# Kernel optimization log

Hardware: AMD Instinct MI355X
Metric: run time of the kernel (lower is better)

Reference implementation:

```python
import jax, jax.numpy as jnp
import numpy as np

N_EMBD = 1024  # C; source scales scores by C**-0.5 (n_embd, not head_size)


def setup_inputs() -> dict:
    key = jax.random.key(0)
    kx, kk, kq, kv = jax.random.split(key, 4)
    B, T, C, H = 8, 2048, N_EMBD, 64
    x = jax.random.normal(kx, (B, T, C), dtype=jnp.float32)
    Wk = jax.random.normal(kk, (C, H), dtype=jnp.float32) * (C ** -0.5)
    Wq = jax.random.normal(kq, (C, H), dtype=jnp.float32) * (C ** -0.5)
    Wv = jax.random.normal(kv, (C, H), dtype=jnp.float32) * (C ** -0.5)
    return {"x": x, "Wk": Wk, "Wq": Wq, "Wv": Wv}


def reference(x, Wk, Wq, Wv):
    B, T, C = x.shape
    k = jnp.einsum('btc,ch->bth', x, Wk)
    q = jnp.einsum('btc,ch->bth', x, Wq)
    v = jnp.einsum('btc,ch->bth', x, Wv)
    # scores scaled by C**-0.5 (faithful to source, which uses n_embd not head_size)
    wei = jnp.einsum('bth,bsh->bts', q, k) * (C ** -0.5)  # [B,T,T]
    causal = jnp.tril(jnp.ones((T, T), dtype=bool))
    wei = jnp.where(causal, wei, -jnp.inf)
    wei = jax.nn.softmax(wei, axis=-1)
    # dropout is identity in eval mode
    out = jnp.einsum('bts,bsh->bth', wei, v)
    return out
```

## Files before the change

### kernel.cpp

```cpp
#include <hip/hip_runtime.h>


#define B_ 8
#define T_ 2048
#define C_ 1024
#define H_ 64
#define BTH (B_ * T_ * H_)

typedef unsigned short u16;
typedef float f32x4 __attribute__((ext_vector_type(4)));
typedef __bf16 bf16x8 __attribute__((ext_vector_type(8)));
#define AS1 __attribute__((address_space(1)))
#define AS3 __attribute__((address_space(3)))

__device__ __forceinline__ u16 f2bf(float f) {
  union { float f; unsigned u; } c; c.f = f;
  unsigned u = c.u;
  return (u16)((u + 0x7FFFu + ((u >> 16) & 1u)) >> 16);
}

__device__ __forceinline__ bf16x8 cvt8(const float4 a, const float4 b) {
  bf16x8 r;
  r[0] = (__bf16)a.x; r[1] = (__bf16)a.y; r[2] = (__bf16)a.z; r[3] = (__bf16)a.w;
  r[4] = (__bf16)b.x; r[5] = (__bf16)b.y; r[6] = (__bf16)b.z; r[7] = (__bf16)b.w;
  return r;
}

__global__ __launch_bounds__(256)
void wpack(const float* __restrict__ Wk, const float* __restrict__ Wq,
           const float* __restrict__ Wv, u16* __restrict__ Wct) {
  const int g  = blockIdx.x;
  const int k0 = blockIdx.y * 64;
  const float* __restrict__ W = (g == 0) ? Wk : (g == 1) ? Wq : Wv;
#pragma unroll
  for (int it = 0; it < 16; ++it) {
    const int idx = it * 256 + threadIdx.x;
    const int kk = k0 + (idx >> 6), h = idx & 63;
    Wct[(size_t)(g * 64 + h) * C_ + kk] = f2bf(W[(size_t)kk * H_ + h]);
  }
}

__global__ __launch_bounds__(256)
void qkv_gemm(const float* __restrict__ x, const u16* __restrict__ Wct,
              u16* __restrict__ ws) {
  __shared__ u16 As[32 * 128];
  const int tid  = threadIdx.x;
  const int wave = tid >> 6, lane = tid & 63;
  const int l15 = lane & 15, quad = lane >> 4;
  const int r0 = blockIdx.x * 32;
  const int srow = tid >> 3, sseg = tid & 7;
  const float* __restrict__ xsrc = x + (size_t)(r0 + srow) * C_ + sseg * 16;
  u16* const wdst0 = As + srow * 128 + ((2 * sseg)     ^ (srow & 15)) * 8;
  u16* const wdst1 = As + srow * 128 + ((2 * sseg + 1) ^ (srow & 15)) * 8;
  const u16* __restrict__ wp = Wct + (size_t)(wave * 48 + l15) * C_ + quad * 8;
  const u16* const ard0 = As + l15 * 128;
  const u16* const ard1 = As + (16 + l15) * 128;
  const f32x4 z = {0.f, 0.f, 0.f, 0.f};
  f32x4 acc[2][3];
#pragma unroll
  for (int m = 0; m < 2; ++m)
#pragma unroll
    for (int ni = 0; ni < 3; ++ni) acc[m][ni] = z;

#pragma unroll 1
  for (int ks = 0; ks < 8; ++ks) {
    const int k0 = ks * 128;
    float4 xa0 = *(const float4*)(xsrc + k0);
    float4 xa1 = *(const float4*)(xsrc + k0 + 4);
    float4 xa2 = *(const float4*)(xsrc + k0 + 8);
    float4 xa3 = *(const float4*)(xsrc + k0 + 12);
    bf16x8 Bf[3][4];
#pragma unroll
    for (int ni = 0; ni < 3; ++ni)
#pragma unroll
      for (int f = 0; f < 4; ++f)
        Bf[ni][f] = *(const bf16x8*)(wp + (size_t)ni * 16 * C_ + k0 + f * 32);
    __syncthreads();
    *(bf16x8*)wdst0 = cvt8(xa0, xa1);
    *(bf16x8*)wdst1 = cvt8(xa2, xa3);
    __syncthreads();
#pragma unroll
    for (int f = 0; f < 4; ++f) {
      const int co = (((4 * f + quad) ^ l15) * 8);
      const bf16x8 a0 = *(const bf16x8*)(ard0 + co);
      const bf16x8 a1 = *(const bf16x8*)(ard1 + co);
#pragma unroll
      for (int ni = 0; ni < 3; ++ni) {
        acc[0][ni] = __builtin_amdgcn_mfma_f32_16x16x32_bf16(a0, Bf[ni][f], acc[0][ni], 0, 0, 0);
        acc[1][ni] = __builtin_amdgcn_mfma_f32_16x16x32_bf16(a1, Bf[ni][f], acc[1][ni], 0, 0, 0);
      }
    }
  }
  const float SCLL = 0.03125f * 1.44269504088896f;
  const int bb = r0 >> 11;
#pragma unroll
  for (int m = 0; m < 2; ++m) {
    const int rowg = r0 + m * 16;
    const int tb = (rowg & 2047) + quad * 4;
#pragma unroll
    for (int ni = 0; ni < 3; ++ni) {
      const int col = wave * 48 + ni * 16 + l15;
      const int g = col >> 6, h = col & 63;
      f32x4 a = acc[m][ni];
      if (g == 1) { a[0] *= SCLL; a[1] *= SCLL; a[2] *= SCLL; a[3] *= SCLL; }
      if (g < 2) {
        u16* op = ws + (size_t)g * BTH + (size_t)(rowg + quad * 4) * H_ + h;
#pragma unroll
        for (int r = 0; r < 4; ++r) op[(size_t)r * H_] = f2bf(a[r]);
      } else {
        uint2 pk;
        pk.x = (unsigned)f2bf(a[0]) | ((unsigned)f2bf(a[1]) << 16);
        pk.y = (unsigned)f2bf(a[2]) | ((unsigned)f2bf(a[3]) << 16);
        *(uint2*)(ws + (size_t)2 * BTH + (size_t)(bb * H_ + h) * T_ + tb) = pk;
      }
    }
  }
}

__global__ __launch_bounds__(256)
void flash(const u16* __restrict__ ws, float* __restrict__ fpart) {
  __shared__ u16 Ks[2][64 * 64];
  __shared__ u16 Vs[2][64 * 64];
  __shared__ __bf16 Pt[4][16 * 72];
  const u16* __restrict__ kg = ws;
  const u16* __restrict__ qg = ws + BTH;
  const u16* __restrict__ vt = ws + (size_t)2 * BTH;
  const int b  = blockIdx.y;
  const int bx = 143 - (int)blockIdx.x;
  int c = 0;
#pragma unroll
  for (int t = 1; t < 8; ++t)
    if (34 * t - 2 * t * t <= bx) c = t;
  const int u = 4 * c + (bx - (34 * c - 2 * c * c));
  const int tid  = threadIdx.x;
  const int wv   = tid >> 6;
  const int lane = tid & 63;
  const int l15  = lane & 15, quad = lane >> 4;
  const int qt   = 4 * u + wv;
  const int t0   = qt * 16;
  const int st0  = 4 * c;
  const int stE  = (st0 + 4 < u + 1) ? st0 + 4 : u + 1;
  const u16* kb0 = kg + (size_t)b * T_ * H_;
  const u16* vb0 = vt + (size_t)b * H_ * T_;
  const int srow = tid >> 3, scp = tid & 7;
  const u16* qrow = qg + ((size_t)(b * T_ + t0 + l15)) * H_ + quad * 8;
  const bf16x8 qf0 = *(const bf16x8*)qrow;
  const bf16x8 qf1 = *(const bf16x8*)(qrow + 32);
  __bf16* pt = &Pt[wv][0];
  const f32x4 z = {0.f, 0.f, 0.f, 0.f};
  f32x4 o[4];
  float lr[4] = {0.f, 0.f, 0.f, 0.f};
#pragma unroll
  for (int hi = 0; hi < 4; ++hi) o[hi] = z;

  {
    const int s00 = st0 * 64;
#pragma unroll
    for (int jj = 0; jj < 2; ++jj) {
      const int row = jj * 32 + srow;
      const int sc  = scp ^ (row & 7);
      __builtin_amdgcn_global_load_lds(
          (const AS1 unsigned*)(kb0 + (size_t)(s00 + row) * H_ + sc * 8),
          (AS3 unsigned*)(&Ks[0][(jj * 256 + tid) * 8]), 16, 0, 0);
      __builtin_amdgcn_global_load_lds(
          (const AS1 unsigned*)(vb0 + (size_t)row * T_ + s00 + sc * 8),
          (AS3 unsigned*)(&Vs[0][(jj * 256 + tid) * 8]), 16, 0, 0);
    }
  }
  __syncthreads();

#pragma unroll 1
  for (int st = st0; st < stE; ++st) {
    const int cur = (st - st0) & 1;
    if (st + 1 < stE) {
      const int s1 = (st + 1) * 64;
#pragma unroll
      for (int jj = 0; jj < 2; ++jj) {
        const int row = jj * 32 + srow;
        const int sc  = scp ^ (row & 7);
        __builtin_amdgcn_global_load_lds(
            (const AS1 unsigned*)(kb0 + (size_t)(s1 + row) * H_ + sc * 8),
            (AS3 unsigned*)(&Ks[cur ^ 1][(jj * 256 + tid) * 8]), 16, 0, 0);
        __builtin_amdgcn_global_load_lds(
            (const AS1 unsigned*)(vb0 + (size_t)row * T_ + s1 + sc * 8),
            (AS3 unsigned*)(&Vs[cur ^ 1][(jj * 256 + tid) * 8]), 16, 0, 0);
      }
    }
    const u16* Kc = &Ks[cur][0];
    const u16* Vc = &Vs[cur][0];
    const int sw = (l15 & 7);
    f32x4 s[4];
#pragma unroll
    for (int ni = 0; ni < 4; ++ni) {
      const u16* kr = Kc + (ni * 16 + l15) * 64;
      const bf16x8 k0 = *(const bf16x8*)(kr + ((quad       ^ sw) * 8));
      const bf16x8 k1 = *(const bf16x8*)(kr + (((4 + quad) ^ sw) * 8));
      s[ni] = __builtin_amdgcn_mfma_f32_16x16x32_bf16(qf0, k0, z, 0, 0, 0);
      s[ni] = __builtin_amdgcn_mfma_f32_16x16x32_bf16(qf1, k1, s[ni], 0, 0, 0);
    }
    if (st == u) {
      const int s0 = st * 64;
#pragma unroll
      for (int ni = 0; ni < 4; ++ni)
#pragma unroll
        for (int r = 0; r < 4; ++r)
          if (s0 + ni * 16 + l15 > t0 + quad * 4 + r) s[ni][r] = -1e30f;
    }
    float p[4][4];
#pragma unroll
    for (int ni = 0; ni < 4; ++ni)
#pragma unroll
      for (int r = 0; r < 4; ++r) p[ni][r] = __builtin_amdgcn_exp2f(s[ni][r]);
#pragma unroll
    for (int r = 0; r < 4; ++r)
      lr[r] += (p[0][r] + p[1][r]) + (p[2][r] + p[3][r]);
#pragma unroll
    for (int ni = 0; ni < 4; ++ni)
#pragma unroll
      for (int r = 0; r < 4; ++r)
        pt[(quad * 4 + r) * 72 + ni * 16 + l15] = (__bf16)p[ni][r];
    asm volatile("s_waitcnt lgkmcnt(0)" ::: "memory");
    const bf16x8 pa0 = *(const bf16x8*)(pt + l15 * 72 + quad * 8);
    const bf16x8 pa1 = *(const bf16x8*)(pt + l15 * 72 + 32 + quad * 8);
    asm volatile("" ::: "memory");
#pragma unroll
    for (int hi = 0; hi < 4; ++hi) {
      const u16* vr = Vc + (hi * 16 + l15) * 64;
      const bf16x8 v0 = *(const bf16x8*)(vr + ((quad       ^ sw) * 8));
      const bf16x8 v1 = *(const bf16x8*)(vr + (((4 + quad) ^ sw) * 8));
      o[hi] = __builtin_amdgcn_mfma_f32_16x16x32_bf16(pa0, v0, o[hi], 0, 0, 0);
      o[hi] = __builtin_amdgcn_mfma_f32_16x16x32_bf16(pa1, v1, o[hi], 0, 0, 0);
    }
    __syncthreads();
  }
#pragma unroll
  for (int d = 1; d < 16; d <<= 1)
#pragma unroll
    for (int r = 0; r < 4; ++r) lr[r] += __shfl_xor(lr[r], d, 64);
  float* po = fpart + (size_t)((b * 128 + qt) * 8 + c) * 1040;
#pragma unroll
  for (int hi = 0; hi < 4; ++hi)
#pragma unroll
    for (int r = 0; r < 4; ++r)
      po[(quad * 4 + r) * 64 + hi * 16 + l15] = o[hi][r];
  if (l15 == 0) {
#pragma unroll
    for (int r = 0; r < 4; ++r) po[1024 + quad * 4 + r] = lr[r];
  }
}

__global__ __launch_bounds__(256)
void freduce(const float* __restrict__ fpart, float* __restrict__ out) {
  const int qt  = blockIdx.x;
  const int b   = blockIdx.y;
  const int tid = threadIdx.x;
  const int nc  = (qt >> 4) + 1;
  const float* __restrict__ pb = fpart + (size_t)(b * 128 + qt) * 8 * 1040;
  __shared__ float ls[16];
  if (tid < 16) {
    float s = 0.f;
#pragma unroll 1
    for (int i = 0; i < nc; ++i) s += pb[(size_t)i * 1040 + 1024 + tid];
    ls[tid] = s;
  }
  __syncthreads();
  f32x4 a = {0.f, 0.f, 0.f, 0.f};
#pragma unroll 1
  for (int i = 0; i < nc; ++i)
    a += *(const f32x4*)(pb + (size_t)i * 1040 + tid * 4);
  const float inv = 1.0f / ls[tid >> 4];
  a[0] *= inv; a[1] *= inv; a[2] *= inv; a[3] *= inv;
  *(f32x4*)(out + (size_t)(b * T_ + qt * 16 + (tid >> 4)) * H_ + ((tid * 4) & 63)) = a;
}

extern "C" void kernel_launch(void* const* d_in, const int* in_sizes, int n_in,
                              void* d_out, int out_size, void* d_ws, size_t ws_size,
                              hipStream_t stream) {
  const float* x  = (const float*)d_in[0];
  const float* Wk = (const float*)d_in[1];
  const float* Wq = (const float*)d_in[2];
  const float* Wv = (const float*)d_in[3];
  u16*   ws  = (u16*)d_ws;
  u16*   Wct = ws + (size_t)3 * BTH;
  float* fpart = (float*)(ws + (size_t)3 * BTH + 192 * 1024);
  float* out = (float*)d_out;
  wpack<<<dim3(3, 16), 256, 0, stream>>>(Wk, Wq, Wv, Wct);
  qkv_gemm<<<dim3(512), 256, 0, stream>>>(x, Wct, ws);
  flash<<<dim3(144, B_), 256, 0, stream>>>(ws, fpart);
  freduce<<<dim3(128, B_), 256, 0, stream>>>(fpart, out);
}
```

Measured before the change: 142.9 us.

## Double-buffer QKV GEMM LDS tile and enlarge row tile to 64

```diff
diff --git a/kernel.cpp b/kernel.cpp
--- a/kernel.cpp
+++ b/kernel.cpp
@@ -25,6 +25,12 @@
   r[4] = (__bf16)b.x; r[5] = (__bf16)b.y; r[6] = (__bf16)b.z; r[7] = (__bf16)b.w;
   return r;
 }
+
+#define GBAR() do {                                        \
+    asm volatile("s_waitcnt lgkmcnt(0)" ::: "memory");     \
+    __builtin_amdgcn_s_barrier();                          \
+    __builtin_amdgcn_sched_barrier(0);                     \
+  } while (0)
 
 __global__ __launch_bounds__(256)
 void wpack(const float* __restrict__ Wk, const float* __restrict__ Wq,
@@ -43,58 +49,106 @@
 __global__ __launch_bounds__(256)
 void qkv_gemm(const float* __restrict__ x, const u16* __restrict__ Wct,
               u16* __restrict__ ws) {
-  __shared__ u16 As[32 * 128];
+  __shared__ u16 As[2][64 * 128];
   const int tid  = threadIdx.x;
   const int wave = tid >> 6, lane = tid & 63;
   const int l15 = lane & 15, quad = lane >> 4;
-  const int r0 = blockIdx.x * 32;
-  const int srow = tid >> 3, sseg = tid & 7;
-  const float* __restrict__ xsrc = x + (size_t)(r0 + srow) * C_ + sseg * 16;
-  u16* const wdst0 = As + srow * 128 + ((2 * sseg)     ^ (srow & 15)) * 8;
-  u16* const wdst1 = As + srow * 128 + ((2 * sseg + 1) ^ (srow & 15)) * 8;
+  const int r0 = blockIdx.x * 64;
+  const int srow = tid >> 2, sseg = tid & 3;
+  const int swz = srow & 15;
+  const float* __restrict__ xsrc = x + (size_t)(r0 + srow) * C_ + sseg * 32;
+  u16* wd0[4]; u16* wd1[4];
+#pragma unroll
+  for (int jj = 0; jj < 4; ++jj) {
+    const int c = ((4 * sseg + jj) ^ swz) * 8;
+    wd0[jj] = &As[0][srow * 128 + c];
+    wd1[jj] = &As[1][srow * 128 + c];
+  }
   const u16* __restrict__ wp = Wct + (size_t)(wave * 48 + l15) * C_ + quad * 8;
-  const u16* const ard0 = As + l15 * 128;
-  const u16* const ard1 = As + (16 + l15) * 128;
   const f32x4 z = {0.f, 0.f, 0.f, 0.f};
-  f32x4 acc[2][3];
-#pragma unroll
-  for (int m = 0; m < 2; ++m)
+  f32x4 acc[4][3];
+#pragma unroll
+  for (int m = 0; m < 4; ++m)
 #pragma unroll
     for (int ni = 0; ni < 3; ++ni) acc[m][ni] = z;
 
-#pragma unroll 1
-  for (int ks = 0; ks < 8; ++ks) {
-    const int k0 = ks * 128;
-    float4 xa0 = *(const float4*)(xsrc + k0);
-    float4 xa1 = *(const float4*)(xsrc + k0 + 4);
-    float4 xa2 = *(const float4*)(xsrc + k0 + 8);
-    float4 xa3 = *(const float4*)(xsrc + k0 + 12);
-    bf16x8 Bf[3][4];
-#pragma unroll
-    for (int ni = 0; ni < 3; ++ni)
-#pragma unroll
-      for (int f = 0; f < 4; ++f)
-        Bf[ni][f] = *(const bf16x8*)(wp + (size_t)ni * 16 * C_ + k0 + f * 32);
-    __syncthreads();
-    *(bf16x8*)wdst0 = cvt8(xa0, xa1);
-    *(bf16x8*)wdst1 = cvt8(xa2, xa3);
-    __syncthreads();
-#pragma unroll
-    for (int f = 0; f < 4; ++f) {
-      const int co = (((4 * f + quad) ^ l15) * 8);
-      const bf16x8 a0 = *(const bf16x8*)(ard0 + co);
-      const bf16x8 a1 = *(const bf16x8*)(ard1 + co);
-#pragma unroll
-      for (int ni = 0; ni < 3; ++ni) {
-        acc[0][ni] = __builtin_amdgcn_mfma_f32_16x16x32_bf16(a0, Bf[ni][f], acc[0][ni], 0, 0, 0);
-        acc[1][ni] = __builtin_amdgcn_mfma_f32_16x16x32_bf16(a1, Bf[ni][f], acc[1][ni], 0, 0, 0);
-      }
+  float4 xA[8], xB[8];
+#pragma unroll
+  for (int j = 0; j < 8; ++j) xA[j] = *(const float4*)(xsrc + j * 4);
+#pragma unroll
+  for (int jj = 0; jj < 4; ++jj)
+    *(bf16x8*)wd0[jj] = cvt8(xA[2 * jj], xA[2 * jj + 1]);
+#pragma unroll
+  for (int j = 0; j < 8; ++j) xB[j] = *(const float4*)(xsrc + 128 + j * 4);
+  GBAR();
+
+#pragma unroll
+  for (int kp = 0; kp < 4; ++kp) {
+    {
+      const int k0 = (2 * kp) * 128;
+      bf16x8 Bf[3][4];
+#pragma unroll
+      for (int ni = 0; ni < 3; ++ni)
+#pragma unroll
+        for (int f = 0; f < 4; ++f)
+          Bf[ni][f] = *(const bf16x8*)(wp + (size_t)ni * 16 * C_ + k0 + f * 32);
+      if (kp < 3) {
+#pragma unroll
+        for (int j = 0; j < 8; ++j)
+          xA[j] = *(const float4*)(xsrc + k0 + 256 + j * 4);
+      }
+#pragma unroll
+      for (int f = 0; f < 4; ++f) {
+        const int co = ((4 * f + quad) ^ l15) * 8;
+#pragma unroll
+        for (int m = 0; m < 4; ++m) {
+          const bf16x8 a = *(const bf16x8*)(&As[0][(m * 16 + l15) * 128 + co]);
+#pragma unroll
+          for (int ni = 0; ni < 3; ++ni)
+            acc[m][ni] = __builtin_amdgcn_mfma_f32_16x16x32_bf16(a, Bf[ni][f], acc[m][ni], 0, 0, 0);
+        }
+      }
+#pragma unroll
+      for (int jj = 0; jj < 4; ++jj)
+        *(bf16x8*)wd1[jj] = cvt8(xB[2 * jj], xB[2 * jj + 1]);
+      GBAR();
+    }
+    {
+      const int k0 = (2 * kp + 1) * 128;
+      bf16x8 Bf[3][4];
+#pragma unroll
+      for (int ni = 0; ni < 3; ++ni)
+#pragma unroll
+        for (int f = 0; f < 4; ++f)
+          Bf[ni][f] = *(const bf16x8*)(wp + (size_t)ni * 16 * C_ + k0 + f * 32);
+      if (kp < 3) {
+#pragma unroll
+        for (int j = 0; j < 8; ++j)
+          xB[j] = *(const float4*)(xsrc + k0 + 256 + j * 4);
+      }
+#pragma unroll
+      for (int f = 0; f < 4; ++f) {
+        const int co = ((4 * f + quad) ^ l15) * 8;
+#pragma unroll
+        for (int m = 0; m < 4; ++m) {
+          const bf16x8 a = *(const bf16x8*)(&As[1][(m * 16 + l15) * 128 + co]);
+#pragma unroll
+          for (int ni = 0; ni < 3; ++ni)
+            acc[m][ni] = __builtin_amdgcn_mfma_f32_16x16x32_bf16(a, Bf[ni][f], acc[m][ni], 0, 0, 0);
+        }
+      }
+      if (kp < 3) {
+#pragma unroll
+        for (int jj = 0; jj < 4; ++jj)
+          *(bf16x8*)wd0[jj] = cvt8(xA[2 * jj], xA[2 * jj + 1]);
+      }
+      GBAR();
     }
   }
   const float SCLL = 0.03125f * 1.44269504088896f;
   const int bb = r0 >> 11;
 #pragma unroll
-  for (int m = 0; m < 2; ++m) {
+  for (int m = 0; m < 4; ++m) {
     const int rowg = r0 + m * 16;
     const int tb = (rowg & 2047) + quad * 4;
 #pragma unroll
@@ -285,7 +339,7 @@
   float* fpart = (float*)(ws + (size_t)3 * BTH + 192 * 1024);
   float* out = (float*)d_out;
   wpack<<<dim3(3, 16), 256, 0, stream>>>(Wk, Wq, Wv, Wct);
-  qkv_gemm<<<dim3(512), 256, 0, stream>>>(x, Wct, ws);
+  qkv_gemm<<<dim3(256), 256, 0, stream>>>(x, Wct, ws);
   flash<<<dim3(144, B_), 256, 0, stream>>>(ws, fpart);
   freduce<<<dim3(128, B_), 256, 0, stream>>>(fpart, out);
 }
```

Measured after the change: 139.9 us. 2.1% less time.

## Drop LDS staging in QKV GEMM, load A fragments directly with register prefetch

Applied to the files above, without the earlier changes.

```diff
diff --git a/kernel.cpp b/kernel.cpp
--- a/kernel.cpp
+++ b/kernel.cpp
@@ -43,76 +43,67 @@
 __global__ __launch_bounds__(256)
 void qkv_gemm(const float* __restrict__ x, const u16* __restrict__ Wct,
               u16* __restrict__ ws) {
-  __shared__ u16 As[32 * 128];
   const int tid  = threadIdx.x;
-  const int wave = tid >> 6, lane = tid & 63;
+  const int wv   = tid >> 6, lane = tid & 63;
   const int l15 = lane & 15, quad = lane >> 4;
-  const int r0 = blockIdx.x * 32;
-  const int srow = tid >> 3, sseg = tid & 7;
-  const float* __restrict__ xsrc = x + (size_t)(r0 + srow) * C_ + sseg * 16;
-  u16* const wdst0 = As + srow * 128 + ((2 * sseg)     ^ (srow & 15)) * 8;
-  u16* const wdst1 = As + srow * 128 + ((2 * sseg + 1) ^ (srow & 15)) * 8;
-  const u16* __restrict__ wp = Wct + (size_t)(wave * 48 + l15) * C_ + quad * 8;
-  const u16* const ard0 = As + l15 * 128;
-  const u16* const ard1 = As + (16 + l15) * 128;
+  const int ch = blockIdx.x & 1;
+  const int mt = (blockIdx.x >> 1) * 4 + wv;
+  const int r0 = mt * 16;
+  const float* __restrict__ xw = x + (size_t)(r0 + l15) * C_ + quad * 8;
+  const u16*   __restrict__ bw = Wct + (size_t)(ch * 96 + l15) * C_ + quad * 8;
   const f32x4 z = {0.f, 0.f, 0.f, 0.f};
-  f32x4 acc[2][3];
-#pragma unroll
-  for (int m = 0; m < 2; ++m)
-#pragma unroll
-    for (int ni = 0; ni < 3; ++ni) acc[m][ni] = z;
-
-#pragma unroll 1
-  for (int ks = 0; ks < 8; ++ks) {
-    const int k0 = ks * 128;
-    float4 xa0 = *(const float4*)(xsrc + k0);
-    float4 xa1 = *(const float4*)(xsrc + k0 + 4);
-    float4 xa2 = *(const float4*)(xsrc + k0 + 8);
-    float4 xa3 = *(const float4*)(xsrc + k0 + 12);
-    bf16x8 Bf[3][4];
-#pragma unroll
-    for (int ni = 0; ni < 3; ++ni)
-#pragma unroll
-      for (int f = 0; f < 4; ++f)
-        Bf[ni][f] = *(const bf16x8*)(wp + (size_t)ni * 16 * C_ + k0 + f * 32);
-    __syncthreads();
-    *(bf16x8*)wdst0 = cvt8(xa0, xa1);
-    *(bf16x8*)wdst1 = cvt8(xa2, xa3);
-    __syncthreads();
-#pragma unroll
-    for (int f = 0; f < 4; ++f) {
-      const int co = (((4 * f + quad) ^ l15) * 8);
-      const bf16x8 a0 = *(const bf16x8*)(ard0 + co);
-      const bf16x8 a1 = *(const bf16x8*)(ard1 + co);
-#pragma unroll
-      for (int ni = 0; ni < 3; ++ni) {
-        acc[0][ni] = __builtin_amdgcn_mfma_f32_16x16x32_bf16(a0, Bf[ni][f], acc[0][ni], 0, 0, 0);
-        acc[1][ni] = __builtin_amdgcn_mfma_f32_16x16x32_bf16(a1, Bf[ni][f], acc[1][ni], 0, 0, 0);
-      }
-    }
-  }
+  f32x4 acc[6];
+#pragma unroll
+  for (int ni = 0; ni < 6; ++ni) acc[ni] = z;
+
+  float4 xa0 = *(const float4*)(xw);
+  float4 xa1 = *(const float4*)(xw + 4);
+  bf16x8 bfc[6];
+#pragma unroll
+  for (int ni = 0; ni < 6; ++ni)
+    bfc[ni] = *(const bf16x8*)(bw + (size_t)ni * 16 * C_);
+
+#pragma unroll 2
+  for (int ks = 0; ks < 32; ++ks) {
+    const int k1 = (ks + 1) * 32;
+    float4 na0, na1;
+    bf16x8 bfn[6];
+    if (ks < 31) {
+      na0 = *(const float4*)(xw + k1);
+      na1 = *(const float4*)(xw + k1 + 4);
+#pragma unroll
+      for (int ni = 0; ni < 6; ++ni)
+        bfn[ni] = *(const bf16x8*)(bw + (size_t)ni * 16 * C_ + k1);
+    }
+    const bf16x8 af = cvt8(xa0, xa1);
+#pragma unroll
+    for (int ni = 0; ni < 6; ++ni)
+      acc[ni] = __builtin_amdgcn_mfma_f32_16x16x32_bf16(af, bfc[ni], acc[ni], 0, 0, 0);
+    if (ks < 31) {
+      xa0 = na0; xa1 = na1;
+#pragma unroll
+      for (int ni = 0; ni < 6; ++ni) bfc[ni] = bfn[ni];
+    }
+  }
+
   const float SCLL = 0.03125f * 1.44269504088896f;
   const int bb = r0 >> 11;
-#pragma unroll
-  for (int m = 0; m < 2; ++m) {
-    const int rowg = r0 + m * 16;
-    const int tb = (rowg & 2047) + quad * 4;
-#pragma unroll
-    for (int ni = 0; ni < 3; ++ni) {
-      const int col = wave * 48 + ni * 16 + l15;
-      const int g = col >> 6, h = col & 63;
-      f32x4 a = acc[m][ni];
-      if (g == 1) { a[0] *= SCLL; a[1] *= SCLL; a[2] *= SCLL; a[3] *= SCLL; }
-      if (g < 2) {
-        u16* op = ws + (size_t)g * BTH + (size_t)(rowg + quad * 4) * H_ + h;
-#pragma unroll
-        for (int r = 0; r < 4; ++r) op[(size_t)r * H_] = f2bf(a[r]);
-      } else {
-        uint2 pk;
-        pk.x = (unsigned)f2bf(a[0]) | ((unsigned)f2bf(a[1]) << 16);
-        pk.y = (unsigned)f2bf(a[2]) | ((unsigned)f2bf(a[3]) << 16);
-        *(uint2*)(ws + (size_t)2 * BTH + (size_t)(bb * H_ + h) * T_ + tb) = pk;
-      }
+  const int tb = (r0 & 2047) + quad * 4;
+#pragma unroll
+  for (int ni = 0; ni < 6; ++ni) {
+    const int col = ch * 96 + ni * 16 + l15;
+    const int g = col >> 6, h = col & 63;
+    f32x4 a = acc[ni];
+    if (g == 1) { a[0] *= SCLL; a[1] *= SCLL; a[2] *= SCLL; a[3] *= SCLL; }
+    if (g < 2) {
+      u16* op = ws + (size_t)g * BTH + (size_t)(r0 + quad * 4) * H_ + h;
+#pragma unroll
+      for (int r = 0; r < 4; ++r) op[(size_t)r * H_] = f2bf(a[r]);
+    } else {
+      uint2 pk;
+      pk.x = (unsigned)f2bf(a[0]) | ((unsigned)f2bf(a[1]) << 16);
+      pk.y = (unsigned)f2bf(a[2]) | ((unsigned)f2bf(a[3]) << 16);
+      *(uint2*)(ws + (size_t)2 * BTH + (size_t)(bb * H_ + h) * T_ + tb) = pk;
     }
   }
 }
```

New measurement: 172.6 us. 1.21x slower.

## Double-buffer QKV GEMM with async LDS weight loads and larger 64-row tiles

Applied to the files above, without the earlier changes.

```diff
diff --git a/kernel.cpp b/kernel.cpp
--- a/kernel.cpp
+++ b/kernel.cpp
@@ -40,21 +40,24 @@
   }
 }
 
-__global__ __launch_bounds__(256)
+__global__ __launch_bounds__(512, 1)
 void qkv_gemm(const float* __restrict__ x, const u16* __restrict__ Wct,
               u16* __restrict__ ws) {
-  __shared__ u16 As[32 * 128];
+  __shared__ u16 Bs[2][192 * 128];
+  __shared__ u16 Xs[2][64 * 128];
   const int tid  = threadIdx.x;
-  const int wave = tid >> 6, lane = tid & 63;
+  const int wv   = tid >> 6, lane = tid & 63;
   const int l15 = lane & 15, quad = lane >> 4;
-  const int r0 = blockIdx.x * 32;
-  const int srow = tid >> 3, sseg = tid & 7;
-  const float* __restrict__ xsrc = x + (size_t)(r0 + srow) * C_ + sseg * 16;
-  u16* const wdst0 = As + srow * 128 + ((2 * sseg)     ^ (srow & 15)) * 8;
-  u16* const wdst1 = As + srow * 128 + ((2 * sseg + 1) ^ (srow & 15)) * 8;
-  const u16* __restrict__ wp = Wct + (size_t)(wave * 48 + l15) * C_ + quad * 8;
-  const u16* const ard0 = As + l15 * 128;
-  const u16* const ard1 = As + (16 + l15) * 128;
+  const int wr = wv >> 2, wc = wv & 3;
+  const int r0 = blockIdx.x * 64;
+  const int xrow = tid >> 3, xcp = tid & 7;
+  const int xw0 = (xcp ^ (xrow & 7)) * 8;
+  const float* __restrict__ xsrc = x + (size_t)(r0 + xrow) * C_;
+  u16* const xd0 = &Xs[0][xrow * 128 + xw0];
+  u16* const xd1 = &Xs[1][xrow * 128 + xw0];
+  const int arow = wr * 32 + l15;
+  const int brow = wc * 48 + l15;
+  const int cksw = (l15 & 7);
   const f32x4 z = {0.f, 0.f, 0.f, 0.f};
   f32x4 acc[2][3];
 #pragma unroll
@@ -62,44 +65,76 @@
 #pragma unroll
     for (int ni = 0; ni < 3; ++ni) acc[m][ni] = z;
 
+  float4 xr[4];
+  xr[0] = *(const float4*)(xsrc + xcp * 8);
+  xr[1] = *(const float4*)(xsrc + xcp * 8 + 4);
+  xr[2] = *(const float4*)(xsrc + (xcp + 8) * 8);
+  xr[3] = *(const float4*)(xsrc + (xcp + 8) * 8 + 4);
+#pragma unroll
+  for (int it = 0; it < 6; ++it) {
+    const int slot = it * 512 + tid;
+    const int row = slot >> 4, cp = slot & 15;
+    const int sc = cp ^ (row & 7);
+    __builtin_amdgcn_global_load_lds(
+        (const AS1 unsigned*)(Wct + (size_t)row * C_ + sc * 8),
+        (AS3 unsigned*)(&Bs[0][slot * 8]), 16, 0, 0);
+  }
+  *(bf16x8*)xd0 = cvt8(xr[0], xr[1]);
+  *(bf16x8*)(xd0 + 64) = cvt8(xr[2], xr[3]);
+  __syncthreads();
+
 #pragma unroll 1
-  for (int ks = 0; ks < 8; ++ks) {
-    const int k0 = ks * 128;
-    float4 xa0 = *(const float4*)(xsrc + k0);
-    float4 xa1 = *(const float4*)(xsrc + k0 + 4);
-    float4 xa2 = *(const float4*)(xsrc + k0 + 8);
-    float4 xa3 = *(const float4*)(xsrc + k0 + 12);
-    bf16x8 Bf[3][4];
-#pragma unroll
-    for (int ni = 0; ni < 3; ++ni)
-#pragma unroll
-      for (int f = 0; f < 4; ++f)
-        Bf[ni][f] = *(const bf16x8*)(wp + (size_t)ni * 16 * C_ + k0 + f * 32);
+  for (int st = 0; st < 8; ++st) {
+    const int cur = st & 1;
+    const int co0 = cur * (64 * 128);
+    const int cb0 = cur * (192 * 128);
+    if (st < 7) {
+      const int k1 = (st + 1) * 128;
+      xr[0] = *(const float4*)(xsrc + k1 + xcp * 8);
+      xr[1] = *(const float4*)(xsrc + k1 + xcp * 8 + 4);
+      xr[2] = *(const float4*)(xsrc + k1 + (xcp + 8) * 8);
+      xr[3] = *(const float4*)(xsrc + k1 + (xcp + 8) * 8 + 4);
+#pragma unroll
+      for (int it = 0; it < 6; ++it) {
+        const int slot = it * 512 + tid;
+        const int row = slot >> 4, cp = slot & 15;
+        const int sc = cp ^ (row & 7);
+        __builtin_amdgcn_global_load_lds(
+            (const AS1 unsigned*)(Wct + (size_t)row * C_ + k1 + sc * 8),
+            (AS3 unsigned*)(&Bs[cur ^ 1][slot * 8]), 16, 0, 0);
+      }
+    }
+    const u16* Xc = &Xs[0][0] + co0;
+    const u16* Bc = &Bs[0][0] + cb0;
+#pragma unroll
+    for (int kk = 0; kk < 4; ++kk) {
+      const int co = (((kk * 4 + quad) ^ cksw)) * 8;
+      const bf16x8 a0 = *(const bf16x8*)(Xc + arow * 128 + co);
+      const bf16x8 a1 = *(const bf16x8*)(Xc + (arow + 16) * 128 + co);
+#pragma unroll
+      for (int ni = 0; ni < 3; ++ni) {
+        const bf16x8 b = *(const bf16x8*)(Bc + (brow + ni * 16) * 128 + co);
+        acc[0][ni] = __builtin_amdgcn_mfma_f32_16x16x32_bf16(a0, b, acc[0][ni], 0, 0, 0);
+        acc[1][ni] = __builtin_amdgcn_mfma_f32_16x16x32_bf16(a1, b, acc[1][ni], 0, 0, 0);
+      }
+    }
+    if (st < 7) {
+      u16* xd = cur ? xd0 : xd1;
+      *(bf16x8*)xd = cvt8(xr[0], xr[1]);
+      *(bf16x8*)(xd + 64) = cvt8(xr[2], xr[3]);
+    }
     __syncthreads();
-    *(bf16x8*)wdst0 = cvt8(xa0, xa1);
-    *(bf16x8*)wdst1 = cvt8(xa2, xa3);
-    __syncthreads();
-#pragma unroll
-    for (int f = 0; f < 4; ++f) {
-      const int co = (((4 * f + quad) ^ l15) * 8);
-      const bf16x8 a0 = *(const bf16x8*)(ard0 + co);
-      const bf16x8 a1 = *(const bf16x8*)(ard1 + co);
-#pragma unroll
-      for (int ni = 0; ni < 3; ++ni) {
-        acc[0][ni] = __builtin_amdgcn_mfma_f32_16x16x32_bf16(a0, Bf[ni][f], acc[0][ni], 0, 0, 0);
-        acc[1][ni] = __builtin_amdgcn_mfma_f32_16x16x32_bf16(a1, Bf[ni][f], acc[1][ni], 0, 0, 0);
-      }
-    }
-  }
+  }
+
   const float SCLL = 0.03125f * 1.44269504088896f;
-  const int bb = r0 >> 11;
 #pragma unroll
   for (int m = 0; m < 2; ++m) {
-    const int rowg = r0 + m * 16;
+    const int rowg = r0 + wr * 32 + m * 16;
+    const int bb = rowg >> 11;
     const int tb = (rowg & 2047) + quad * 4;
 #pragma unroll
     for (int ni = 0; ni < 3; ++ni) {
-      const int col = wave * 48 + ni * 16 + l15;
+      const int col = wc * 48 + ni * 16 + l15;
       const int g = col >> 6, h = col & 63;
       f32x4 a = acc[m][ni];
       if (g == 1) { a[0] *= SCLL; a[1] *= SCLL; a[2] *= SCLL; a[3] *= SCLL; }
@@ -285,7 +320,7 @@
   float* fpart = (float*)(ws + (size_t)3 * BTH + 192 * 1024);
   float* out = (float*)d_out;
   wpack<<<dim3(3, 16), 256, 0, stream>>>(Wk, Wq, Wv, Wct);
-  qkv_gemm<<<dim3(512), 256, 0, stream>>>(x, Wct, ws);
+  qkv_gemm<<<dim3(256), 512, 0, stream>>>(x, Wct, ws);
   flash<<<dim3(144, B_), 256, 0, stream>>>(ws, fpart);
   freduce<<<dim3(128, B_), 256, 0, stream>>>(fpart, out);
 }
```

New measurement: 134.7 us. 1.06x faster.
